# Kernel tuning notes

Measured on AMD Instinct MI355X. Metric: run time of the kernel, lower is better.

## Reference

```python
import jax, jax.numpy as jnp
import numpy as np

EMBED_DIM = 256
NUM_HEADS = 8
HEAD_DIM = EMBED_DIM // NUM_HEADS
SCALE = float(np.sqrt(HEAD_DIM))


def setup_inputs() -> dict:
    key = jax.random.key(0)
    ks = jax.random.split(key, 9)
    B, C, H, W = 4, EMBED_DIM, 48, 48
    s = 1.0 / np.sqrt(C)
    x = jax.random.normal(ks[0], (B, C, H, W), dtype=jnp.float32)
    # 1x1 convs == per-pixel channel matmuls; store as [out_c, in_c] weights + bias
    wq = jax.random.normal(ks[1], (C, C), dtype=jnp.float32) * s
    wk = jax.random.normal(ks[2], (C, C), dtype=jnp.float32) * s
    wv = jax.random.normal(ks[3], (C, C), dtype=jnp.float32) * s
    wo = jax.random.normal(ks[4], (C, C), dtype=jnp.float32) * s
    bq = jax.random.normal(ks[5], (C,), dtype=jnp.float32) * s
    bk = jax.random.normal(ks[6], (C,), dtype=jnp.float32) * s
    bv = jax.random.normal(ks[7], (C,), dtype=jnp.float32) * s
    bo = jax.random.normal(ks[8], (C,), dtype=jnp.float32) * s
    return {"x": x, "wq": wq, "bq": bq, "wk": wk, "bk": bk,
            "wv": wv, "bv": bv, "wo": wo, "bo": bo}


def reference(x, wq, bq, wk, bk, wv, bv, wo, bo):
    B, C, H, W = x.shape
    L = H * W
    xf = x.reshape(B, C, L)  # [B, C, L]
    def proj(w, b):
        y = jnp.einsum('oc,bcl->bol', w, xf) + b[None, :, None]
        return y.reshape(B, NUM_HEADS, HEAD_DIM, L)
    q = proj(wq, bq)  # [B, h, d, L]
    k = proj(wk, bk)
    v = proj(wv, bv)
    # scores: [B, h, Lq, Lk]
    attn = jnp.einsum('bhdq,bhdk->bhqk', q, k) / SCALE
    attn = jax.nn.softmax(attn, axis=-1)
    # dropout is identity in eval mode
    out = jnp.einsum('bhdk,bhqk->bhdq', v, attn)  # [B, h, d, L]
    out = out.reshape(B, C, L)
    out = jnp.einsum('oc,bcl->bol', wo, out) + bo[None, :, None]
    return out.reshape(B, C, H, W)
```

## Files before the change

kernel.cpp:

```cpp
#include <hip/hip_runtime.h>
#include <hip/hip_bf16.h>

typedef __attribute__((ext_vector_type(8))) short bf16x8;
typedef __attribute__((ext_vector_type(4))) float f32x4;
typedef __attribute__((ext_vector_type(16))) float f32x16;

#define DEV static __device__ __forceinline__

constexpr int Cc = 256;
constexpr int Ll = 2304;
constexpr float SM_C = 0.25503486f;

#if __has_builtin(__builtin_amdgcn_exp2f)
#define EXP2(x) __builtin_amdgcn_exp2f(x)
#else
#define EXP2(x) exp2f(x)
#endif
#if __has_builtin(__builtin_amdgcn_rcpf)
#define RCP(x) __builtin_amdgcn_rcpf(x)
#else
#define RCP(x) (1.0f / (x))
#endif

DEV unsigned short f2bf(float f) {
  union { float f; unsigned u; } v; v.f = f;
  unsigned r = v.u + 0x7FFFu + ((v.u >> 16) & 1u);
  return (unsigned short)(r >> 16);
}

DEV unsigned short f2bfc(float f) {
  union { __hip_bfloat16 h; unsigned short u; } c;
  c.h = __float2bfloat16(f);
  return c.u;
}

DEV unsigned packbf(float lo, float hi) {
  return (unsigned)f2bfc(lo) | ((unsigned)f2bfc(hi) << 16);
}

__global__ __launch_bounds__(256) void k_wconv(
    const float* __restrict__ wq, const float* __restrict__ wk,
    const float* __restrict__ wv, const float* __restrict__ wo,
    unsigned short* __restrict__ wb) {
  int m = blockIdx.y;
  const float* src = (m == 0) ? wq : (m == 1) ? wk : (m == 2) ? wv : wo;
  float sc = (m == 0) ? SM_C : 1.0f;
  int i = (blockIdx.x * 256 + threadIdx.x) * 8;
  float4 f0 = *(const float4*)&src[i];
  float4 f1 = *(const float4*)&src[i + 4];
  uint4 o;
  o.x = (unsigned)f2bf(f0.x * sc) | ((unsigned)f2bf(f0.y * sc) << 16);
  o.y = (unsigned)f2bf(f0.z * sc) | ((unsigned)f2bf(f0.w * sc) << 16);
  o.z = (unsigned)f2bf(f1.x * sc) | ((unsigned)f2bf(f1.y * sc) << 16);
  o.w = (unsigned)f2bf(f1.z * sc) | ((unsigned)f2bf(f1.w * sc) << 16);
  *(uint4*)&wb[(size_t)m * 65536 + i] = o;
}

__global__ __launch_bounds__(256) void k_xpose(const float* __restrict__ x,
                                               unsigned short* __restrict__ xt) {
  int b = blockIdx.z;
  int c0 = blockIdx.y * 32;
  int l = blockIdx.x * 256 + threadIdx.x;
  const float* xp = x + (size_t)b * Cc * Ll + l;
  unsigned short* op = xt + ((size_t)b * Ll + l) * Cc + c0;
  float v[32];
#pragma unroll
  for (int j = 0; j < 32; ++j) v[j] = xp[(size_t)(c0 + j) * Ll];
  unsigned u[16];
#pragma unroll
  for (int j = 0; j < 16; ++j)
    u[j] = (unsigned)f2bf(v[2 * j]) | ((unsigned)f2bf(v[2 * j + 1]) << 16);
  uint4* o4 = (uint4*)op;
#pragma unroll
  for (int j = 0; j < 4; ++j)
    o4[j] = make_uint4(u[4 * j], u[4 * j + 1], u[4 * j + 2], u[4 * j + 3]);
}

__global__ __launch_bounds__(256) void k_qkv(
    const unsigned short* __restrict__ xt, const unsigned short* __restrict__ wb,
    const float* __restrict__ bq, const float* __restrict__ bk,
    const float* __restrict__ bv,
    unsigned short* __restrict__ qt, unsigned short* __restrict__ kt,
    unsigned short* __restrict__ vm) {
  __shared__ __align__(16) unsigned short Bs[64][264];
  int b = blockIdx.z;
  int m0 = blockIdx.y * 64, n0 = blockIdx.x * 64;
  int tid = threadIdx.x, lane = tid & 63, wave = tid >> 6;
  int g = lane >> 4, cl = lane & 15;
  const uint4* bp = (const uint4*)(xt + ((size_t)b * Ll + n0) * 256);
#pragma unroll
  for (int j = 0; j < 8; ++j) {
    int idx = j * 256 + tid;
    *(uint4*)&Bs[idx >> 5][(idx & 31) * 8] = bp[idx];
  }
  __syncthreads();
  int ob = m0 + wave * 16 + g * 4;
  int h = ob >> 5, d0 = ob & 31;
#pragma unroll
  for (int p = 0; p < 3; ++p) {
    const unsigned short* Wrow =
        wb + (size_t)p * 65536 + (size_t)(m0 + wave * 16 + cl) * 256 + g * 8;
    bf16x8 af[8];
#pragma unroll
    for (int ks = 0; ks < 8; ++ks) af[ks] = *(const bf16x8*)&Wrow[ks * 32];
    f32x4 acc[4] = {};
#pragma unroll
    for (int ks = 0; ks < 8; ++ks) {
#pragma unroll
      for (int nf = 0; nf < 4; ++nf) {
        bf16x8 bb = *(const bf16x8*)&Bs[nf * 16 + cl][ks * 32 + g * 8];
        acc[nf] = __builtin_amdgcn_mfma_f32_16x16x32_bf16(af[ks], bb, acc[nf], 0, 0, 0);
      }
    }
    const float* bias = (p == 0) ? bq : (p == 1) ? bk : bv;
    float sc = (p == 0) ? SM_C : 1.0f;
    float b0 = bias[ob] * sc, b1 = bias[ob + 1] * sc;
    float b2 = bias[ob + 2] * sc, b3 = bias[ob + 3] * sc;
#pragma unroll
    for (int nf = 0; nf < 4; ++nf) {
      int l = n0 + nf * 16 + cl;
      float v0 = acc[nf][0] + b0, v1 = acc[nf][1] + b1;
      float v2 = acc[nf][2] + b2, v3 = acc[nf][3] + b3;
      if (p < 2) {
        unsigned short* dst = ((p == 0) ? qt : kt) +
            ((size_t)(b * 8 + h) * Ll + l) * 32 + d0;
        *(uint2*)dst = make_uint2(packbf(v0, v1), packbf(v2, v3));
      } else {
        int lp = n0 + nf * 16 + ((cl & 3) | ((cl & 4) << 1) | ((cl & 8) >> 1));
        size_t base = (size_t)(b * 8 + h) * 32 + d0;
        vm[(base + 0) * Ll + lp] = f2bfc(v0);
        vm[(base + 1) * Ll + lp] = f2bfc(v1);
        vm[(base + 2) * Ll + lp] = f2bfc(v2);
        vm[(base + 3) * Ll + lp] = f2bfc(v3);
      }
    }
  }
}

DEV void attn_step(uint4 k0, uint4 k1, uint4 k2, uint4 k3,
                   uint4 v0, uint4 v1, uint4 v2, uint4 v3,
                   bf16x8 qf0, bf16x8 qf1, bf16x8 ones,
                   f32x16& oacc, f32x16& osum) {
  union U { uint4 u; bf16x8 v; };
  U a0{k0}, a1{k1}, a2{k2}, a3{k3}, w0{v0}, w1{v1}, w2{v2}, w3{v3};
  f32x16 p0 = {}, p1 = {};
  p0 = __builtin_amdgcn_mfma_f32_32x32x16_bf16(a0.v, qf0, p0, 0, 0, 0);
  p0 = __builtin_amdgcn_mfma_f32_32x32x16_bf16(a1.v, qf1, p0, 0, 0, 0);
  p1 = __builtin_amdgcn_mfma_f32_32x32x16_bf16(a2.v, qf0, p1, 0, 0, 0);
  p1 = __builtin_amdgcn_mfma_f32_32x32x16_bf16(a3.v, qf1, p1, 0, 0, 0);
#pragma unroll
  for (int r = 0; r < 16; ++r) { p0[r] = EXP2(p0[r]); p1[r] = EXP2(p1[r]); }
  union { unsigned w[16]; bf16x8 v8[4]; } Wp;
#pragma unroll
  for (int m = 0; m < 8; ++m) {
    Wp.w[m] = packbf(p0[2 * m], p0[2 * m + 1]);
    Wp.w[8 + m] = packbf(p1[2 * m], p1[2 * m + 1]);
  }
  oacc = __builtin_amdgcn_mfma_f32_32x32x16_bf16(Wp.v8[0], w0.v, oacc, 0, 0, 0);
  osum = __builtin_amdgcn_mfma_f32_32x32x16_bf16(Wp.v8[0], ones, osum, 0, 0, 0);
  oacc = __builtin_amdgcn_mfma_f32_32x32x16_bf16(Wp.v8[1], w1.v, oacc, 0, 0, 0);
  osum = __builtin_amdgcn_mfma_f32_32x32x16_bf16(Wp.v8[1], ones, osum, 0, 0, 0);
  oacc = __builtin_amdgcn_mfma_f32_32x32x16_bf16(Wp.v8[2], w2.v, oacc, 0, 0, 0);
  osum = __builtin_amdgcn_mfma_f32_32x32x16_bf16(Wp.v8[2], ones, osum, 0, 0, 0);
  oacc = __builtin_amdgcn_mfma_f32_32x32x16_bf16(Wp.v8[3], w3.v, oacc, 0, 0, 0);
  osum = __builtin_amdgcn_mfma_f32_32x32x16_bf16(Wp.v8[3], ones, osum, 0, 0, 0);
}

#define LDK(d0, d1, d2, d3, J)                              \
  d0 = *(const uint4*)(kl0 + ((J) * 64 + 0) * 32 + 0);      \
  d1 = *(const uint4*)(kl0 + ((J) * 64 + 0) * 32 + 16);     \
  d2 = *(const uint4*)(kl0 + ((J) * 64 + 32) * 32 + 0);     \
  d3 = *(const uint4*)(kl0 + ((J) * 64 + 32) * 32 + 16);
#define LDV(d0, d1, d2, d3, J)                  \
  d0 = *(const uint4*)(vl0 + (J) * 64 + 0);     \
  d1 = *(const uint4*)(vl0 + (J) * 64 + 16);    \
  d2 = *(const uint4*)(vl0 + (J) * 64 + 32);    \
  d3 = *(const uint4*)(vl0 + (J) * 64 + 48);

__global__ __launch_bounds__(64, 3) void k_attn(
    const unsigned short* __restrict__ qt,
    const unsigned short* __restrict__ kt,
    const unsigned short* __restrict__ vp,
    unsigned short* __restrict__ aot) {
  int n = blockIdx.x;
  int bh = n & 31, qw = n >> 5;
  int b = bh >> 3, h = bh & 7;
  int lane = threadIdx.x;
  int hi = lane >> 5, c = lane & 31;

  const unsigned short* qb = qt + (size_t)bh * Ll * 32;
  const unsigned short* kl0 = kt + (size_t)bh * Ll * 32 + (size_t)c * 32 + hi * 8;
  const unsigned short* vl0 = vp + (size_t)bh * 32 * Ll + (size_t)c * Ll + hi * 8;

  bf16x8 qf0 = *(const bf16x8*)&qb[(size_t)(qw * 32 + c) * 32 + hi * 8];
  bf16x8 qf1 = *(const bf16x8*)&qb[(size_t)(qw * 32 + c) * 32 + 16 + hi * 8];

  bf16x8 ones;
#pragma unroll
  for (int i = 0; i < 8; ++i) ones[i] = (short)0x3F80;

  f32x16 oacc = {}, osum = {};

  uint4 ka0, ka1, ka2, ka3, kb0, kb1, kb2, kb3, va0, va1, va2, va3;
  LDK(ka0, ka1, ka2, ka3, 0);
  for (int j = 0; j < 36; j += 2) {
    LDV(va0, va1, va2, va3, j);
    LDK(kb0, kb1, kb2, kb3, j + 1);
    attn_step(ka0, ka1, ka2, ka3, va0, va1, va2, va3, qf0, qf1, ones, oacc, osum);
    LDV(va0, va1, va2, va3, j + 1);
    if (j + 2 < 36) { LDK(ka0, ka1, ka2, ka3, j + 2); }
    attn_step(kb0, kb1, kb2, kb3, va0, va1, va2, va3, qf0, qf1, ones, oacc, osum);
  }

  unsigned short* ob = aot + ((size_t)b * Ll + (size_t)qw * 32) * 256 + h * 32 + c;
#pragma unroll
  for (int r = 0; r < 16; ++r) {
    int qrl = (r & 3) + 8 * (r >> 2) + 4 * hi;
    ob[(size_t)qrl * 256] = f2bfc(oacc[r] * RCP(osum[r]));
  }
}

__global__ __launch_bounds__(256) void k_oproj(
    const unsigned short* __restrict__ aot, const unsigned short* __restrict__ wb,
    const float* __restrict__ bo, float* __restrict__ out) {
  __shared__ __align__(16) unsigned short Bs[64][264];
  int b = blockIdx.z;
  int m0 = blockIdx.y * 64, n0 = blockIdx.x * 64;
  int tid = threadIdx.x, lane = tid & 63, wave = tid >> 6;
  int g = lane >> 4, cl = lane & 15;
  const uint4* bp = (const uint4*)(aot + ((size_t)b * Ll + n0) * 256);
#pragma unroll
  for (int j = 0; j < 8; ++j) {
    int idx = j * 256 + tid;
    *(uint4*)&Bs[idx >> 5][(idx & 31) * 8] = bp[idx];
  }
  __syncthreads();
  const unsigned short* Wrow =
      wb + (size_t)3 * 65536 + (size_t)(m0 + wave * 16 + cl) * 256 + g * 8;
  bf16x8 af[8];
#pragma unroll
  for (int ks = 0; ks < 8; ++ks) af[ks] = *(const bf16x8*)&Wrow[ks * 32];
  f32x4 acc[4] = {};
#pragma unroll
  for (int ks = 0; ks < 8; ++ks) {
#pragma unroll
    for (int nf = 0; nf < 4; ++nf) {
      bf16x8 bb = *(const bf16x8*)&Bs[nf * 16 + cl][ks * 32 + g * 8];
      acc[nf] = __builtin_amdgcn_mfma_f32_16x16x32_bf16(af[ks], bb, acc[nf], 0, 0, 0);
    }
  }
  int ob = m0 + wave * 16 + g * 4;
  float b0 = bo[ob], b1 = bo[ob + 1], b2 = bo[ob + 2], b3 = bo[ob + 3];
#pragma unroll
  for (int nf = 0; nf < 4; ++nf) {
    int l = n0 + nf * 16 + cl;
    float* dst = out + ((size_t)b * 256 + ob) * Ll + l;
    dst[(size_t)0 * Ll] = acc[nf][0] + b0;
    dst[(size_t)1 * Ll] = acc[nf][1] + b1;
    dst[(size_t)2 * Ll] = acc[nf][2] + b2;
    dst[(size_t)3 * Ll] = acc[nf][3] + b3;
  }
}

extern "C" void kernel_launch(void* const* d_in, const int* in_sizes, int n_in,
                              void* d_out, int out_size, void* d_ws, size_t ws_size,
                              hipStream_t stream) {
  (void)in_sizes; (void)n_in; (void)out_size; (void)ws_size;
  const float* x  = (const float*)d_in[0];
  const float* wq = (const float*)d_in[1];
  const float* bq = (const float*)d_in[2];
  const float* wk = (const float*)d_in[3];
  const float* bk = (const float*)d_in[4];
  const float* wv = (const float*)d_in[5];
  const float* bv = (const float*)d_in[6];
  const float* wo = (const float*)d_in[7];
  const float* bo = (const float*)d_in[8];
  float* out = (float*)d_out;

  const size_t CH = (size_t)4 * Ll * Cc;
  unsigned short* xt = (unsigned short*)d_ws;
  unsigned short* qt = xt + CH;
  unsigned short* kt = xt + 2 * CH;
  unsigned short* vm = xt + 3 * CH;
  unsigned short* wbq = xt + 4 * CH;
  unsigned short* aot = xt;

  k_wconv<<<dim3(32, 4), 256, 0, stream>>>(wq, wk, wv, wo, wbq);
  k_xpose<<<dim3(9, 8, 4), 256, 0, stream>>>(x, xt);
  k_qkv<<<dim3(36, 4, 4), 256, 0, stream>>>(xt, wbq, bq, bk, bv, qt, kt, vm);
  k_attn<<<dim3(2304), 64, 0, stream>>>(qt, kt, vm, aot);
  k_oproj<<<dim3(36, 4, 4), 256, 0, stream>>>(aot, wbq, bo, out);
}
```

Baseline: 164.0 us.

## Split attention key range across two waves per query tile and reduce via LDS

Result: slower. 170.7 us (+4.1%).

```diff
diff --git a/kernel.cpp b/kernel.cpp
--- a/kernel.cpp
+++ b/kernel.cpp
@@ -177,23 +177,29 @@
   d2 = *(const uint4*)(vl0 + (J) * 64 + 32);    \
   d3 = *(const uint4*)(vl0 + (J) * 64 + 48);
 
-__global__ __launch_bounds__(64, 3) void k_attn(
+__global__ __launch_bounds__(256) void k_attn(
     const unsigned short* __restrict__ qt,
     const unsigned short* __restrict__ kt,
     const unsigned short* __restrict__ vp,
     unsigned short* __restrict__ aot) {
+  __shared__ float Osh[2][32][33];
+  __shared__ float Ssh[2][32];
   int n = blockIdx.x;
-  int bh = n & 31, qw = n >> 5;
+  int bh = n & 31, q64 = n >> 5;
   int b = bh >> 3, h = bh & 7;
-  int lane = threadIdx.x;
+  int tid = threadIdx.x, wave = tid >> 6, lane = tid & 63;
+  int qsub = wave >> 1, sstr = wave & 1;
   int hi = lane >> 5, c = lane & 31;
 
   const unsigned short* qb = qt + (size_t)bh * Ll * 32;
-  const unsigned short* kl0 = kt + (size_t)bh * Ll * 32 + (size_t)c * 32 + hi * 8;
-  const unsigned short* vl0 = vp + (size_t)bh * 32 * Ll + (size_t)c * Ll + hi * 8;
-
-  bf16x8 qf0 = *(const bf16x8*)&qb[(size_t)(qw * 32 + c) * 32 + hi * 8];
-  bf16x8 qf1 = *(const bf16x8*)&qb[(size_t)(qw * 32 + c) * 32 + 16 + hi * 8];
+  const unsigned short* kl0 = kt + (size_t)bh * Ll * 32 +
+      (size_t)(sstr * 18 * 64) * 32 + (size_t)c * 32 + hi * 8;
+  const unsigned short* vl0 = vp + (size_t)bh * 32 * Ll + (size_t)c * Ll +
+      sstr * 18 * 64 + hi * 8;
+
+  int qrow0 = q64 * 64 + qsub * 32;
+  bf16x8 qf0 = *(const bf16x8*)&qb[(size_t)(qrow0 + c) * 32 + hi * 8];
+  bf16x8 qf1 = *(const bf16x8*)&qb[(size_t)(qrow0 + c) * 32 + 16 + hi * 8];
 
   bf16x8 ones;
 #pragma unroll
@@ -203,20 +209,33 @@
 
   uint4 ka0, ka1, ka2, ka3, kb0, kb1, kb2, kb3, va0, va1, va2, va3;
   LDK(ka0, ka1, ka2, ka3, 0);
-  for (int j = 0; j < 36; j += 2) {
+  for (int j = 0; j < 18; j += 2) {
     LDV(va0, va1, va2, va3, j);
     LDK(kb0, kb1, kb2, kb3, j + 1);
     attn_step(ka0, ka1, ka2, ka3, va0, va1, va2, va3, qf0, qf1, ones, oacc, osum);
     LDV(va0, va1, va2, va3, j + 1);
-    if (j + 2 < 36) { LDK(ka0, ka1, ka2, ka3, j + 2); }
+    if (j + 2 < 18) { LDK(ka0, ka1, ka2, ka3, j + 2); }
     attn_step(kb0, kb1, kb2, kb3, va0, va1, va2, va3, qf0, qf1, ones, oacc, osum);
   }
 
-  unsigned short* ob = aot + ((size_t)b * Ll + (size_t)qw * 32) * 256 + h * 32 + c;
-#pragma unroll
-  for (int r = 0; r < 16; ++r) {
-    int qrl = (r & 3) + 8 * (r >> 2) + 4 * hi;
-    ob[(size_t)qrl * 256] = f2bfc(oacc[r] * RCP(osum[r]));
+  if (sstr == 1) {
+#pragma unroll
+    for (int r = 0; r < 16; ++r) {
+      int qrl = (r & 3) + 8 * (r >> 2) + 4 * hi;
+      Osh[qsub][qrl][c] = oacc[r];
+      if (c == 0) Ssh[qsub][qrl] = osum[r];
+    }
+  }
+  __syncthreads();
+  if (sstr == 0) {
+    unsigned short* ob = aot + ((size_t)b * Ll + qrow0) * 256 + h * 32 + c;
+#pragma unroll
+    for (int r = 0; r < 16; ++r) {
+      int qrl = (r & 3) + 8 * (r >> 2) + 4 * hi;
+      float ot = oacc[r] + Osh[qsub][qrl][c];
+      float st = osum[r] + Ssh[qsub][qrl];
+      ob[(size_t)qrl * 256] = f2bfc(ot * RCP(st));
+    }
   }
 }
 
@@ -288,6 +307,6 @@
   k_wconv<<<dim3(32, 4), 256, 0, stream>>>(wq, wk, wv, wo, wbq);
   k_xpose<<<dim3(9, 8, 4), 256, 0, stream>>>(x, xt);
   k_qkv<<<dim3(36, 4, 4), 256, 0, stream>>>(xt, wbq, bq, bk, bv, qt, kt, vm);
-  k_attn<<<dim3(2304), 64, 0, stream>>>(qt, kt, vm, aot);
+  k_attn<<<dim3(1152), 256, 0, stream>>>(qt, kt, vm, aot);
   k_oproj<<<dim3(36, 4, 4), 256, 0, stream>>>(aot, wbq, bo, out);
 }
```
